# Kernel optimization log

Measured on AMD Instinct MI355X. Metric: run time of the kernel, lower is better.

## Reference

```python
import jax, jax.numpy as jnp
import numpy as np

NUM_CLASSES = 91
BBOX_XFORM_CLIP = float(np.log(1000.0 / 16.0))
WX, WY, WW, WH = 10.0, 10.0, 5.0, 5.0  # torchvision BoxCoder weights
DETECTIONS_PER_IMG = 100


def _decode_boxes(reg, props):
    # reg: [P, 4*C], props: [P, 4] -> [P, C, 4]  (torchvision BoxCoder.decode)
    widths = props[:, 2] - props[:, 0]
    heights = props[:, 3] - props[:, 1]
    ctr_x = props[:, 0] + 0.5 * widths
    ctr_y = props[:, 1] + 0.5 * heights
    r = reg.reshape(reg.shape[0], -1, 4)
    dx = r[..., 0] / WX
    dy = r[..., 1] / WY
    dw = jnp.minimum(r[..., 2] / WW, BBOX_XFORM_CLIP)
    dh = jnp.minimum(r[..., 3] / WH, BBOX_XFORM_CLIP)
    pcx = dx * widths[:, None] + ctr_x[:, None]
    pcy = dy * heights[:, None] + ctr_y[:, None]
    pw = jnp.exp(dw) * widths[:, None]
    ph = jnp.exp(dh) * heights[:, None]
    return jnp.stack([pcx - 0.5 * pw, pcy - 0.5 * ph, pcx + 0.5 * pw, pcy + 0.5 * ph], axis=-1)


def _clip_boxes(boxes, h, w):
    x = jnp.clip(boxes[..., 0::2], 0.0, float(w))
    y = jnp.clip(boxes[..., 1::2], 0.0, float(h))
    return jnp.stack([x[..., 0], y[..., 0], x[..., 1], y[..., 1]], axis=-1)


def setup_inputs() -> dict:
    key = jax.random.key(0)
    k1, k2, k3, k4, k5 = jax.random.split(key, 5)
    B, P, C, FD = 8, 4096, NUM_CLASSES, 1024
    N = B * P
    class_logits = jax.random.normal(k1, (N, C), dtype=jnp.float32)
    box_regression = 0.5 * jax.random.normal(k2, (N, 4 * C), dtype=jnp.float32)
    # valid proposal boxes inside an 800x800 image: x1<x2, y1<y2
    xy = jax.random.uniform(k3, (N, 2), dtype=jnp.float32) * 700.0
    wh = jax.random.uniform(k4, (N, 2), dtype=jnp.float32) * 96.0 + 4.0
    proposals = jnp.concatenate([xy, xy + wh], axis=-1)
    box_features = jax.random.normal(k5, (N, FD), dtype=jnp.float32)
    return {"class_logits": class_logits, "box_regression": box_regression,
            "proposals": proposals, "box_features": box_features,
            "batch_size": B, "image_h": 800, "image_w": 800}


def reference(class_logits, box_regression, proposals, box_features, batch_size, image_h, image_w):
    B = int(batch_size)
    N = class_logits.shape[0]
    P = N // B
    lg = class_logits.reshape(B, P, NUM_CLASSES)
    rg = box_regression.reshape(B, P, 4 * NUM_CLASSES)
    pr = proposals.reshape(B, P, 4)
    ft = box_features.reshape(B, P, -1)

    def per_image(lg_i, rg_i, pr_i, ft_i):
        boxes = _decode_boxes(rg_i, pr_i)            # [P, C, 4]
        scores = jax.nn.softmax(lg_i, axis=-1)       # [P, C]
        boxes = _clip_boxes(boxes, image_h, image_w)
        boxes = boxes[:, 1:].reshape(-1, 4)          # drop background class -> [P*(C-1), 4]
        scores = scores[:, 1:].reshape(-1)
        # batched_nms with iou_threshold=1.0 never suppresses anything (IoU<=1 always),
        # so keep == indices sorted by score descending, truncated to detections_per_img.
        keep = jnp.argsort(-scores)[:DETECTIONS_PER_IMG]
        boxes = boxes / float(image_h)               # source divides by image_shape[0] only
        kept_boxes = boxes[keep]                     # [D, 4]
        feat_idx = keep // (NUM_CLASSES - 1)         # source: keep / (num_classes-1) int div
        kept_feats = ft_i[feat_idx]                  # [D, FD]
        return kept_boxes, kept_feats

    all_boxes, all_features = jax.vmap(per_image)(lg, rg, pr, ft)
    return all_boxes, all_features
```

## Files before the change

kernel.cpp:

```cpp
#include <hip/hip_runtime.h>
#include <hip/hip_bf16.h>

#define NCLS 91
#define NFG 90
#define NDET 100
#define FDIM 1024
#define CAP 4096
#define NBUK 4096
#define BBOX_CLIP 4.135166556742356f
#define K1_TPB 256
#define RPB 32
#define K2_TPB 1024

__global__ __launch_bounds__(K1_TPB) void k1_soft(
        const float* __restrict__ logits, float* __restrict__ rowoff,
        unsigned* __restrict__ maxk, int N) {
    int wave = threadIdx.x >> 6, lane = threadIdx.x & 63;
    int rowbase = blockIdx.x * RPB + wave * (RPB / 4);
    for (int it = 0; it < RPB / 4; it++) {
        long long row = rowbase + it;
        if (row >= N) return;
        const float* r = logits + row * NCLS;
        float l1 = r[lane];
        float l2 = (lane < NCLS - 64) ? r[64 + lane] : -INFINITY;
        float mf = fmaxf((lane == 0) ? -INFINITY : l1, l2);
        #pragma unroll
        for (int o = 32; o; o >>= 1) mf = fmaxf(mf, __shfl_xor(mf, o));
        float m = fmaxf(mf, __shfl(l1, 0));
        float e = expf(l1 - m) + ((lane < NCLS - 64) ? expf(l2 - m) : 0.0f);
        #pragma unroll
        for (int o = 32; o; o >>= 1) e += __shfl_xor(e, o);
        float off = m + logf(e);
        unsigned km = __float_as_uint(expf(mf - off));
        if (lane == 0) { rowoff[row] = off; maxk[row] = km; }
    }
}

__device__ __forceinline__ void find_threshold(const unsigned* hist,
                                               unsigned* wsum, unsigned* sh_lb,
                                               int tid, unsigned target) {
    unsigned local[16]; unsigned s = 0, run = 0;
    if (tid < 256) {
        #pragma unroll
        for (int i = 0; i < 16; i++) { local[i] = hist[tid * 16 + i]; s += local[i]; }
        run = s;
        #pragma unroll
        for (int off = 1; off < 64; off <<= 1) {
            unsigned v = __shfl_down(run, off);
            if ((tid & 63) + off < 64) run += v;
        }
        if ((tid & 63) == 0) wsum[tid >> 6] = run;
    }
    __syncthreads();
    if (tid < 256) {
        int w = tid >> 6;
        #pragma unroll
        for (int ww = 0; ww < 4; ww++) if (ww > w) run += wsum[ww];
        unsigned above = run - s;
        #pragma unroll
        for (int i = 15; i >= 0; i--) {
            unsigned prev = above; above += local[i];
            if (above >= target && prev < target)
                *sh_lb = ((unsigned)(tid * 16 + i)) << 20;
        }
    }
    __syncthreads();
}

__global__ __launch_bounds__(K2_TPB) void k2_select(
        const float* __restrict__ logits, const float* __restrict__ reg,
        const float* __restrict__ props,
        const int* __restrict__ pH, const int* __restrict__ pW,
        const float* __restrict__ rowoff, const unsigned* __restrict__ maxk,
        float* __restrict__ outBoxes, unsigned* __restrict__ keepRow, int P) {
    __shared__ unsigned long long cand[CAP];
    __shared__ unsigned long long cbuf[2048];
    __shared__ unsigned hist[NBUK];
    __shared__ unsigned wsum[4];
    __shared__ unsigned sh_lb, sh_lb2, sh_nhot, sh_ncand, sh_n2;

    const int img = blockIdx.x;
    const int tid = threadIdx.x;
    const unsigned* mk = maxk + (size_t)img * P;
    unsigned* hot = (unsigned*)cbuf;

    if (tid == 0) { sh_nhot = 0; sh_ncand = 0; sh_n2 = 0; sh_lb = 0; sh_lb2 = 0; }
    for (int b = tid; b < NBUK; b += K2_TPB) hist[b] = 0u;
    __syncthreads();

    for (int r = tid; r < P; r += K2_TPB) atomicAdd(&hist[mk[r] >> 20], 1u);
    __syncthreads();
    find_threshold(hist, wsum, &sh_lb, tid, NDET);
    const unsigned lb = sh_lb;
    const unsigned lbh = lb ? lb - 1 : 0;

    for (int r = tid; r < P; r += K2_TPB)
        if (mk[r] >= lbh) hot[atomicAdd(&sh_nhot, 1u)] = (unsigned)r;
    __syncthreads();
    const int nhot = (int)sh_nhot;

    const int wave = tid >> 6, lane = tid & 63;
    for (int i = wave; i < nhot; i += K2_TPB / 64) {
        int rl = (int)hot[i];
        long long row = (long long)img * P + rl;
        float off = rowoff[row];
        const float* r = logits + row * NCLS;
        float l1 = r[lane];
        float l2 = (lane < NCLS - 64) ? r[64 + lane] : -INFINITY;
        if (lane >= 1) {
            unsigned k = __float_as_uint(expf(l1 - off));
            if (k >= lb) {
                unsigned pos = atomicAdd(&sh_ncand, 1u);
                if (pos < CAP)
                    cand[pos] = ((unsigned long long)k << 32) |
                                (unsigned)(0xFFFFFFFFu - (unsigned)(rl * NFG + lane - 1));
            }
        }
        if (lane < NCLS - 64) {
            unsigned k = __float_as_uint(expf(l2 - off));
            if (k >= lb) {
                unsigned pos = atomicAdd(&sh_ncand, 1u);
                if (pos < CAP)
                    cand[pos] = ((unsigned long long)k << 32) |
                                (unsigned)(0xFFFFFFFFu - (unsigned)(rl * NFG + 63 + lane));
            }
        }
    }
    __syncthreads();
    unsigned cnt = sh_ncand; if (cnt > CAP) cnt = CAP;
    int n;

    if (cnt > 128) {
        for (int b = tid; b < NBUK; b += K2_TPB) hist[b] = 0u;
        __syncthreads();
        for (int i = tid; i < (int)cnt; i += K2_TPB)
            atomicAdd(&hist[(unsigned)(cand[i] >> 52)], 1u);
        __syncthreads();
        find_threshold(hist, wsum, &sh_lb2, tid, NDET);
        unsigned lb2 = sh_lb2;
        for (int i = tid; i < (int)cnt; i += K2_TPB) {
            unsigned long long k64 = cand[i];
            if ((unsigned)(k64 >> 32) >= lb2) {
                unsigned pos = atomicAdd(&sh_n2, 1u);
                if (pos < 2048) cbuf[pos] = k64;
            }
        }
        __syncthreads();
        unsigned cnt2 = sh_n2;
        if (cnt2 <= 2048) {
            cnt = cnt2;
            n = 128; while (n < (int)cnt) n <<= 1;
            for (int i = tid; i < n; i += K2_TPB)
                cand[i] = (i < (int)cnt) ? cbuf[i] : 0ULL;
            __syncthreads();
        } else {
            n = 128; while (n < (int)cnt) n <<= 1;
            for (int i = tid; i < n; i += K2_TPB) if (i >= (int)cnt) cand[i] = 0ULL;
            __syncthreads();
        }
    } else {
        n = 128;
        for (int i = tid; i < n; i += K2_TPB) if (i >= (int)cnt) cand[i] = 0ULL;
        __syncthreads();
    }

    for (int k = 2; k <= n; k <<= 1) {
        for (int j = k >> 1; j > 0; j >>= 1) {
            for (int i = tid; i < n; i += K2_TPB) {
                int ixj = i ^ j;
                if (ixj > i) {
                    bool up = ((i & k) == 0);
                    unsigned long long a = cand[i], b = cand[ixj];
                    if ((a > b) == up) { cand[i] = b; cand[ixj] = a; }
                }
            }
            __syncthreads();
        }
    }

    if (tid < NDET) {
        unsigned long long key = cand[n - 1 - tid];
        unsigned e = 0xFFFFFFFFu - (unsigned)(key & 0xFFFFFFFFull);
        int pr = e / NFG, cm = e - pr * NFG, c = cm + 1;
        long long rw = (long long)img * P + pr;
        float x1 = props[rw * 4 + 0], y1 = props[rw * 4 + 1];
        float x2 = props[rw * 4 + 2], y2 = props[rw * 4 + 3];
        float w = x2 - x1, hgt = y2 - y1;
        float cx = x1 + 0.5f * w, cy = y1 + 0.5f * hgt;
        const float* rr = reg + rw * (4 * NCLS) + 4 * c;
        float dx = rr[0] / 10.0f, dy = rr[1] / 10.0f;
        float dw = fminf(rr[2] / 5.0f, BBOX_CLIP);
        float dh = fminf(rr[3] / 5.0f, BBOX_CLIP);
        float pcx = dx * w + cx, pcy = dy * hgt + cy;
        float pw_ = expf(dw) * w, ph_ = expf(dh) * hgt;
        float bx1 = pcx - 0.5f * pw_, by1 = pcy - 0.5f * ph_;
        float bx2 = pcx + 0.5f * pw_, by2 = pcy + 0.5f * ph_;
        float W = (float)(*pW), H = (float)(*pH);
        bx1 = fminf(fmaxf(bx1, 0.0f), W);
        bx2 = fminf(fmaxf(bx2, 0.0f), W);
        by1 = fminf(fmaxf(by1, 0.0f), H);
        by2 = fminf(fmaxf(by2, 0.0f), H);
        int o = (img * NDET + tid) * 4;
        outBoxes[o + 0] = bx1 / H;
        outBoxes[o + 1] = by1 / H;
        outBoxes[o + 2] = bx2 / H;
        outBoxes[o + 3] = by2 / H;
        keepRow[img * NDET + tid] = (unsigned)rw;
    }
}

__global__ __launch_bounds__(256) void k3_feats(
        const float* __restrict__ feats, const unsigned* __restrict__ keepRow,
        float* __restrict__ outF) {
    int det = blockIdx.x;
    long long r = keepRow[det];
    const float4* src = (const float4*)(feats + r * FDIM);
    float4* dst = (float4*)(outF + (long long)det * FDIM);
    dst[threadIdx.x] = src[threadIdx.x];
}

extern "C" void kernel_launch(void* const* d_in, const int* in_sizes, int n_in,
                              void* d_out, int out_size, void* d_ws, size_t ws_size,
                              hipStream_t stream) {
    const float* logits = (const float*)d_in[0];
    const float* reg    = (const float*)d_in[1];
    const float* props  = (const float*)d_in[2];
    const float* feats  = (const float*)d_in[3];
    const int*   pH     = (const int*)d_in[5];
    const int*   pW     = (const int*)d_in[6];

    int N = in_sizes[0] / NCLS;
    int B = out_size / (NDET * (4 + FDIM));
    int P = N / B;

    char* ws = (char*)d_ws;
    float*    rowoff  = (float*)ws;
    unsigned* maxk    = (unsigned*)(rowoff + N);
    unsigned* keepRow = (unsigned*)(maxk + N);

    float* outBoxes = (float*)d_out;
    float* outFeats = outBoxes + (size_t)B * NDET * 4;

    k1_soft<<<(N + RPB - 1) / RPB, K1_TPB, 0, stream>>>(logits, rowoff, maxk, N);
    k2_select<<<B, K2_TPB, 0, stream>>>(logits, reg, props, pH, pW,
                                        rowoff, maxk, outBoxes, keepRow, P);
    k3_feats<<<B * NDET, 256, 0, stream>>>(feats, keepRow, outFeats);
}
```

Before: 224.2 us.

## Replace bitonic sort with rank-based top-k selection and aggregate histogram atomics

The shared-memory bitonic sort of the candidate pool is replaced by a rank computation: each wave counts how many candidates are larger than one candidate and writes it directly to its rank slot if the rank is below 100. This removes the many synchronised sort passes. The row-max histogram build now groups lanes with equal buckets through ballots, so one atomic is issued per distinct bucket per wave. The rank step costs O(n^2) comparisons, which is expensive if the candidate pool is large. Keys are unique, so ranks are distinct.

```diff
diff --git a/kernel.cpp b/kernel.cpp
--- a/kernel.cpp
+++ b/kernel.cpp
@@ -1,5 +1,4 @@
 #include <hip/hip_runtime.h>
-#include <hip/hip_bf16.h>
 
 #define NCLS 91
 #define NFG 90
@@ -76,6 +75,7 @@
     __shared__ unsigned long long cand[CAP];
     __shared__ unsigned long long cbuf[2048];
     __shared__ unsigned hist[NBUK];
+    __shared__ unsigned long long win[NDET];
     __shared__ unsigned wsum[4];
     __shared__ unsigned sh_lb, sh_lb2, sh_nhot, sh_ncand, sh_n2;
 
@@ -88,7 +88,23 @@
     for (int b = tid; b < NBUK; b += K2_TPB) hist[b] = 0u;
     __syncthreads();
 
-    for (int r = tid; r < P; r += K2_TPB) atomicAdd(&hist[mk[r] >> 20], 1u);
+    {
+        const int lane = tid & 63;
+        for (int r = tid; r < P + (K2_TPB - 1); r += K2_TPB) {
+            unsigned b = (r < P) ? (mk[r] >> 20) : 0xFFFFFFFFu;
+            bool done = (r >= P);
+            while (true) {
+                unsigned long long m = __ballot(!done);
+                if (!m) break;
+                int leader = __ffsll((long long)m) - 1;
+                unsigned lb_ = __shfl(b, leader);
+                bool mine = (!done && b == lb_);
+                unsigned long long grp = __ballot(mine);
+                if (lane == leader) atomicAdd(&hist[lb_], (unsigned)__popcll(grp));
+                if (mine) done = true;
+            }
+        }
+    }
     __syncthreads();
     find_threshold(hist, wsum, &sh_lb, tid, NDET);
     const unsigned lb = sh_lb;
@@ -128,7 +144,9 @@
     }
     __syncthreads();
     unsigned cnt = sh_ncand; if (cnt > CAP) cnt = CAP;
-    int n;
+
+    const unsigned long long* pool = cand;
+    unsigned pcnt = cnt;
 
     if (cnt > 128) {
         for (int b = tid; b < NBUK; b += K2_TPB) hist[b] = 0u;
@@ -147,39 +165,22 @@
         }
         __syncthreads();
         unsigned cnt2 = sh_n2;
-        if (cnt2 <= 2048) {
-            cnt = cnt2;
-            n = 128; while (n < (int)cnt) n <<= 1;
-            for (int i = tid; i < n; i += K2_TPB)
-                cand[i] = (i < (int)cnt) ? cbuf[i] : 0ULL;
-            __syncthreads();
-        } else {
-            n = 128; while (n < (int)cnt) n <<= 1;
-            for (int i = tid; i < n; i += K2_TPB) if (i >= (int)cnt) cand[i] = 0ULL;
-            __syncthreads();
-        }
-    } else {
-        n = 128;
-        for (int i = tid; i < n; i += K2_TPB) if (i >= (int)cnt) cand[i] = 0ULL;
-        __syncthreads();
-    }
-
-    for (int k = 2; k <= n; k <<= 1) {
-        for (int j = k >> 1; j > 0; j >>= 1) {
-            for (int i = tid; i < n; i += K2_TPB) {
-                int ixj = i ^ j;
-                if (ixj > i) {
-                    bool up = ((i & k) == 0);
-                    unsigned long long a = cand[i], b = cand[ixj];
-                    if ((a > b) == up) { cand[i] = b; cand[ixj] = a; }
-                }
-            }
-            __syncthreads();
-        }
-    }
+        if (cnt2 <= 2048) { pool = cbuf; pcnt = cnt2; }
+    }
+
+    for (unsigned i = wave; i < pcnt; i += K2_TPB / 64) {
+        unsigned long long me = pool[i];
+        unsigned ng = 0;
+        for (unsigned j = lane; j < pcnt; j += 64)
+            ng += (pool[j] > me) ? 1u : 0u;
+        #pragma unroll
+        for (int o = 32; o; o >>= 1) ng += __shfl_xor(ng, o);
+        if (lane == 0 && ng < NDET) win[ng] = me;
+    }
+    __syncthreads();
 
     if (tid < NDET) {
-        unsigned long long key = cand[n - 1 - tid];
+        unsigned long long key = win[tid];
         unsigned e = 0xFFFFFFFFu - (unsigned)(key & 0xFFFFFFFFull);
         int pr = e / NFG, cm = e - pr * NFG, c = cm + 1;
         long long rw = (long long)img * P + pr;
```

Result: slower. 231.6 us (+3.3%).
